# Performance work log

Hardware: AMD Instinct MI355X
Metric: run time of the kernel (lower is better)

The kernel has to match this reference:

```python
import jax, jax.numpy as jnp
import numpy as np

B, S, D, H = 32, 512, 512, 8
DH = D // H
EXP_FF, EXP_CONV, K = 4, 2, 31
EPS = 1e-5


def _layernorm(x, g, b):
    m = jnp.mean(x, axis=-1, keepdims=True)
    v = jnp.mean(jnp.square(x - m), axis=-1, keepdims=True)
    return (x - m) * jax.lax.rsqrt(v + EPS) * g + b


def _sinusoid_pe(s, d):
    pos = np.arange(s, dtype=np.float32)[:, None]
    i = np.arange(0, d, 2, dtype=np.float32)[None, :]
    ang = pos / np.power(10000.0, i / d)
    pe = np.zeros((s, d), dtype=np.float32)
    pe[:, 0::2] = np.sin(ang)
    pe[:, 1::2] = np.cos(ang)
    return jnp.asarray(pe)


def _rel_shift(ps):
    # Transformer-XL relative shift on [b,h,s,s]
    b, h, s1, s2 = ps.shape
    p = jnp.pad(ps, ((0, 0), (0, 0), (0, 0), (1, 0)))
    p = p.reshape(b, h, s2 + 1, s1)
    return p[:, :, 1:].reshape(b, h, s1, s2)


def setup_inputs() -> dict:
    key = jax.random.key(0)
    ks = iter(jax.random.split(key, 64))
    nrm = lambda shape, sc=0.02: jax.random.normal(next(ks), shape, jnp.float32) * sc
    ones = lambda n: jnp.ones((n,), jnp.float32)
    zeros = lambda n: jnp.zeros((n,), jnp.float32)
    return {
        'x': jax.random.normal(next(ks), (B, S, D), jnp.float32),
        'ff1_g': ones(D), 'ff1_b': zeros(D),
        'ff1_w1': nrm((D, EXP_FF * D)), 'ff1_b1': zeros(EXP_FF * D),
        'ff1_w2': nrm((EXP_FF * D, D)), 'ff1_b2': zeros(D),
        'attn_g': ones(D), 'attn_b': zeros(D),
        'wq': nrm((D, D)), 'bq': zeros(D),
        'wk': nrm((D, D)), 'bk': zeros(D),
        'wv': nrm((D, D)), 'bv': zeros(D),
        'wpos': nrm((D, D)),
        'u_bias': nrm((H, DH)), 'v_bias': nrm((H, DH)),
        'wo': nrm((D, D)), 'bo': zeros(D),
        'conv_g': ones(D), 'conv_b': zeros(D),
        'pw1_w': nrm((D, EXP_CONV * D)), 'pw1_b': zeros(EXP_CONV * D),
        'dw_w': nrm((D, 1, K)),
        'bn_g': ones(D), 'bn_b': zeros(D), 'bn_m': zeros(D), 'bn_v': ones(D),
        'pw2_w': nrm((D, D)), 'pw2_b': zeros(D),
        'ff2_g': ones(D), 'ff2_b': zeros(D),
        'ff2_w1': nrm((D, EXP_FF * D)), 'ff2_b1': zeros(EXP_FF * D),
        'ff2_w2': nrm((EXP_FF * D, D)), 'ff2_b2': zeros(D),
        'ln_g': ones(D), 'ln_b': zeros(D),
    }


def _ff(x, g, b, w1, b1, w2, b2):
    y = _layernorm(x, g, b)
    return jnp.dot(jax.nn.silu(jnp.dot(y, w1) + b1), w2) + b2


def reference(x, ff1_g, ff1_b, ff1_w1, ff1_b1, ff1_w2, ff1_b2,
              attn_g, attn_b, wq, bq, wk, bk, wv, bv, wpos, u_bias, v_bias, wo, bo,
              conv_g, conv_b, pw1_w, pw1_b, dw_w, bn_g, bn_b, bn_m, bn_v, pw2_w, pw2_b,
              ff2_g, ff2_b, ff2_w1, ff2_b1, ff2_w2, ff2_b2, ln_g, ln_b):
    b, s, d = x.shape
    # Macaron FF 1 (half-step residual)
    out = x + 0.5 * _ff(x, ff1_g, ff1_b, ff1_w1, ff1_b1, ff1_w2, ff1_b2)
    # Relative-position multi-head self-attention
    y = _layernorm(out, attn_g, attn_b)
    pe = _sinusoid_pe(s, d)
    q = (jnp.dot(y, wq) + bq).reshape(b, s, H, DH)
    k = (jnp.dot(y, wk) + bk).reshape(b, s, H, DH)
    v = (jnp.dot(y, wv) + bv).reshape(b, s, H, DH)
    p = jnp.dot(pe, wpos).reshape(s, H, DH)
    content = jnp.einsum('bqhd,bkhd->bhqk', q + u_bias, k)
    pos = _rel_shift(jnp.einsum('bqhd,khd->bhqk', q + v_bias, p))
    attn = jax.nn.softmax((content + pos) / np.sqrt(d).astype(np.float32), axis=-1)
    ctx = jnp.einsum('bhqk,bkhd->bqhd', attn, v).reshape(b, s, d)
    out = out + (jnp.dot(ctx, wo) + bo)
    y = _layernorm(out, conv_g, conv_b)
    y = jnp.dot(y, pw1_w) + pw1_b                     # [b,s,2d]
    a, gate = jnp.split(y, 2, axis=-1)
    y = (a * jax.nn.sigmoid(gate)).transpose(0, 2, 1)  # [b,d,s]
    pad = (K - 1) // 2
    y = jax.lax.conv_general_dilated(y, dw_w, (1,), [(pad, pad)],
                                     dimension_numbers=('NCH', 'OIH', 'NCH'),
                                     feature_group_count=d)
    y = (y - bn_m[None, :, None]) * jax.lax.rsqrt(bn_v + EPS)[None, :, None] \
        * bn_g[None, :, None] + bn_b[None, :, None]
    y = jax.nn.silu(y).transpose(0, 2, 1)             # [b,s,d]
    out = out + (jnp.dot(y, pw2_w) + pw2_b)
    # Macaron FF 2 + final LN
    out = out + 0.5 * _ff(out, ff2_g, ff2_b, ff2_w1, ff2_b1, ff2_w2, ff2_b2)
    out = _layernorm(out, ln_g, ln_b)
    return out, attn
```

## Files before the change

kernel.cpp:

```cpp
#include <hip/hip_runtime.h>
#include <cstddef>
#include <cstdint>

#define EPSF 1e-5f

constexpr int BB = 32, SS = 512, DD = 512, HH = 8, DH = 64;
constexpr int NTOK = BB * SS;
constexpr size_t ND = (size_t)NTOK * DD;

typedef __attribute__((ext_vector_type(8))) short bf16x8;
typedef __attribute__((ext_vector_type(4))) float f32x4;

__device__ __forceinline__ float sigmf(float v) { return 1.f / (1.f + __expf(-v)); }

__device__ __forceinline__ ushort f2bf(float f) {
  union { float f; uint32_t u; } x{f};
  uint32_t r = x.u + 0x7FFF + ((x.u >> 16) & 1);
  return (ushort)(r >> 16);
}
__device__ __forceinline__ float bf2f(ushort u) {
  union { uint32_t u; float f; } x{(uint32_t)u << 16};
  return x.f;
}

__device__ __forceinline__ void gload16(const ushort* g, ushort* ldsbase) {
  __builtin_amdgcn_global_load_lds((const __attribute__((address_space(1))) void*)g,
                                   (__attribute__((address_space(3))) void*)ldsbase, 16, 0, 0);
}

__device__ __forceinline__ void xcd_swz(int& bx, int& by) {
  const int gx = gridDim.x;
  const int nwg = gx * gridDim.y;
  const int cpx = nwg >> 3;
  int id = by * gx + bx;
  id = (id & 7) * cpx + (id >> 3);
  bx = id % gx;
  by = id / gx;
}

__device__ __forceinline__ int pswz(int idx) {
  return idx ^ (((idx >> 11) & 3) << 4);
}

__global__ __launch_bounds__(256) void ln_f32(const float* __restrict__ x,
                                              const float* __restrict__ g,
                                              const float* __restrict__ b,
                                              float* __restrict__ y) {
  const int lane = threadIdx.x & 63;
  const int row = blockIdx.x * 4 + (threadIdx.x >> 6);
  const float* xr = x + (size_t)row * 512;
  const float4 v0 = *(const float4*)&xr[lane << 2];
  const float4 v1 = *(const float4*)&xr[256 + (lane << 2)];
  float s = v0.x + v0.y + v0.z + v0.w + v1.x + v1.y + v1.z + v1.w;
#pragma unroll
  for (int o = 32; o > 0; o >>= 1) s += __shfl_xor(s, o);
  const float mean = s * (1.f / 512.f);
  float q = 0.f;
  q += (v0.x - mean) * (v0.x - mean); q += (v0.y - mean) * (v0.y - mean);
  q += (v0.z - mean) * (v0.z - mean); q += (v0.w - mean) * (v0.w - mean);
  q += (v1.x - mean) * (v1.x - mean); q += (v1.y - mean) * (v1.y - mean);
  q += (v1.z - mean) * (v1.z - mean); q += (v1.w - mean) * (v1.w - mean);
#pragma unroll
  for (int o = 32; o > 0; o >>= 1) q += __shfl_xor(q, o);
  const float rs = rsqrtf(q * (1.f / 512.f) + EPSF);
  const float4 g0 = *(const float4*)&g[lane << 2];
  const float4 g1 = *(const float4*)&g[256 + (lane << 2)];
  const float4 b0 = *(const float4*)&b[lane << 2];
  const float4 b1 = *(const float4*)&b[256 + (lane << 2)];
  float* yr = y + (size_t)row * 512;
  float4 o0, o1;
  o0.x = (v0.x - mean) * rs * g0.x + b0.x; o0.y = (v0.y - mean) * rs * g0.y + b0.y;
  o0.z = (v0.z - mean) * rs * g0.z + b0.z; o0.w = (v0.w - mean) * rs * g0.w + b0.w;
  o1.x = (v1.x - mean) * rs * g1.x + b1.x; o1.y = (v1.y - mean) * rs * g1.y + b1.y;
  o1.z = (v1.z - mean) * rs * g1.z + b1.z; o1.w = (v1.w - mean) * rs * g1.w + b1.w;
  *(float4*)&yr[lane << 2] = o0;
  *(float4*)&yr[256 + (lane << 2)] = o1;
}

__global__ __launch_bounds__(256) void ln_bf16(const float* __restrict__ x,
                                               const float* __restrict__ g,
                                               const float* __restrict__ b,
                                               ushort* __restrict__ y) {
  const int lane = threadIdx.x & 63;
  const int row = blockIdx.x * 4 + (threadIdx.x >> 6);
  const float* xr = x + (size_t)row * 512;
  const float4 v0 = *(const float4*)&xr[lane << 2];
  const float4 v1 = *(const float4*)&xr[256 + (lane << 2)];
  float s = v0.x + v0.y + v0.z + v0.w + v1.x + v1.y + v1.z + v1.w;
#pragma unroll
  for (int o = 32; o > 0; o >>= 1) s += __shfl_xor(s, o);
  const float mean = s * (1.f / 512.f);
  float q = 0.f;
  q += (v0.x - mean) * (v0.x - mean); q += (v0.y - mean) * (v0.y - mean);
  q += (v0.z - mean) * (v0.z - mean); q += (v0.w - mean) * (v0.w - mean);
  q += (v1.x - mean) * (v1.x - mean); q += (v1.y - mean) * (v1.y - mean);
  q += (v1.z - mean) * (v1.z - mean); q += (v1.w - mean) * (v1.w - mean);
#pragma unroll
  for (int o = 32; o > 0; o >>= 1) q += __shfl_xor(q, o);
  const float rs = rsqrtf(q * (1.f / 512.f) + EPSF);
  const float4 g0 = *(const float4*)&g[lane << 2];
  const float4 g1 = *(const float4*)&g[256 + (lane << 2)];
  const float4 b0 = *(const float4*)&b[lane << 2];
  const float4 b1 = *(const float4*)&b[256 + (lane << 2)];
  ushort* yr = y + (size_t)row * 512;
  ushort4 o0, o1;
  o0.x = f2bf((v0.x - mean) * rs * g0.x + b0.x); o0.y = f2bf((v0.y - mean) * rs * g0.y + b0.y);
  o0.z = f2bf((v0.z - mean) * rs * g0.z + b0.z); o0.w = f2bf((v0.w - mean) * rs * g0.w + b0.w);
  o1.x = f2bf((v1.x - mean) * rs * g1.x + b1.x); o1.y = f2bf((v1.y - mean) * rs * g1.y + b1.y);
  o1.z = f2bf((v1.z - mean) * rs * g1.z + b1.z); o1.w = f2bf((v1.w - mean) * rs * g1.w + b1.w);
  *(ushort4*)&yr[lane << 2] = o0;
  *(ushort4*)&yr[256 + (lane << 2)] = o1;
}

struct TpArgs {
  const float* src[11];
  ushort* dst[11];
  int K[11];
  int N[11];
  int base[12];
};

__global__ __launch_bounds__(256) void transpose_all(TpArgs a) {
  __shared__ float tile[32][33];
  int s = 0;
  const int bid = blockIdx.x;
  while (s < 10 && bid >= a.base[s + 1]) ++s;
  const int r = bid - a.base[s];
  const int K = a.K[s], N = a.N[s];
  const int ntx = N >> 5;
  const int n0 = (r % ntx) << 5;
  const int k0 = (r / ntx) << 5;
  const float* in = a.src[s];
  ushort* out = a.dst[s];
  const int tx = threadIdx.x & 31, ty = threadIdx.x >> 5;
#pragma unroll
  for (int i = 0; i < 32; i += 8)
    tile[ty + i][tx] = in[(size_t)(k0 + ty + i) * N + n0 + tx];
  __syncthreads();
#pragma unroll
  for (int i = 0; i < 32; i += 8)
    out[(size_t)(n0 + ty + i) * K + k0 + tx] = f2bf(tile[tx][ty + i]);
}

template <int ACT, int RES, int HB, int OBF>
__global__ __launch_bounds__(256) void gemm_bf16(const ushort* __restrict__ A,
                                                 const ushort* __restrict__ Wt,
                                                 const float* __restrict__ bias,
                                                 const float* __restrict__ res,
                                                 void* __restrict__ Cv,
                                                 int M, int K, int N) {
  __shared__ ushort Al[2][8192];
  __shared__ ushort Bl[2][8192];
  const int t = threadIdx.x;
  const int lane = t & 63;
  const int w = t >> 6;
  const int wr = (w >> 1) << 6, wc = (w & 1) << 6;
  int bx = blockIdx.x, by = blockIdx.y;
  xcd_swz(bx, by);
  const int m0 = by << 7, n0 = bx << 7;
  const int lm = lane & 15;
  const int grow = lane >> 3;
  const int gcol = (lane & 7) << 3;

  f32x4 acc[4][4];
#pragma unroll
  for (int i = 0; i < 4; ++i)
#pragma unroll
    for (int j = 0; j < 4; ++j) acc[i][j] = (f32x4)(0.f);

  const int NT = K >> 6;
#pragma unroll
  for (int i = 0; i < 4; ++i) {
    const int s = (w << 2) + i;
    gload16(A + (size_t)(m0 + (s << 3) + grow) * K + gcol, &Al[0][s << 9]);
    gload16(Wt + (size_t)(n0 + (s << 3) + grow) * K + gcol, &Bl[0][s << 9]);
  }
  __syncthreads();
  int cur = 0;
  for (int tt = 0; tt < NT; ++tt) {
    if (tt + 1 < NT) {
      const int k0 = (tt + 1) << 6;
#pragma unroll
      for (int i = 0; i < 4; ++i) {
        const int s = (w << 2) + i;
        gload16(A + (size_t)(m0 + (s << 3) + grow) * K + k0 + gcol, &Al[cur ^ 1][s << 9]);
        gload16(Wt + (size_t)(n0 + (s << 3) + grow) * K + k0 + gcol, &Bl[cur ^ 1][s << 9]);
      }
    }
#pragma unroll
    for (int ks = 0; ks < 2; ++ks) {
      const int kof = (ks << 5) + ((lane >> 4) << 3);
      bf16x8 af[4], bfr[4];
#pragma unroll
      for (int i = 0; i < 4; ++i) af[i] = *(const bf16x8*)&Al[cur][(wr + (i << 4) + lm) * 64 + kof];
#pragma unroll
      for (int j = 0; j < 4; ++j) bfr[j] = *(const bf16x8*)&Bl[cur][(wc + (j << 4) + lm) * 64 + kof];
#pragma unroll
      for (int i = 0; i < 4; ++i)
#pragma unroll
        for (int j = 0; j < 4; ++j)
          acc[i][j] = __builtin_amdgcn_mfma_f32_16x16x32_bf16(af[i], bfr[j], acc[i][j], 0, 0, 0);
    }
    __syncthreads();
    cur ^= 1;
  }

  float bb[4] = {0.f, 0.f, 0.f, 0.f};
  if (HB) {
#pragma unroll
    for (int j = 0; j < 4; ++j) bb[j] = bias[n0 + wc + j * 16 + lm];
  }
  const int rbase = m0 + wr + ((lane >> 4) << 2);
#pragma unroll
  for (int i = 0; i < 4; ++i) {
#pragma unroll
    for (int r = 0; r < 4; ++r) {
      const size_t row = (size_t)(rbase + i * 16 + r);
#pragma unroll
      for (int j = 0; j < 4; ++j) {
        const int col = n0 + wc + j * 16 + lm;
        float v = acc[i][j][r] + bb[j];
        if (ACT == 1) v = v * sigmf(v);
        if (RES == 1) v += res[row * N + col];
        else if (RES == 2) v = res[row * N + col] + 0.5f * v;
        if (OBF) ((ushort*)Cv)[row * N + col] = f2bf(v);
        else ((float*)Cv)[row * N + col] = v;
      }
    }
  }
}

__global__ __launch_bounds__(256) void gemm_qkv(const ushort* __restrict__ A,
                                                const ushort* __restrict__ Wt,
                                                const float* __restrict__ bq,
                                                const float* __restrict__ bk,
                                                const float* __restrict__ bv,
                                                const float* __restrict__ ub,
                                                const float* __restrict__ vb,
                                                ushort* __restrict__ qu,
                                                ushort* __restrict__ qv,
                                                ushort* __restrict__ kbb,
                                                ushort* __restrict__ vT,
                                                int M, int K) {
  __shared__ ushort Al[2][8192];
  __shared__ ushort Bl[2][8192];
  const int t = threadIdx.x;
  const int lane = t & 63;
  const int w = t >> 6;
  const int wr = (w >> 1) << 6, wc = (w & 1) << 6;
  int bx = blockIdx.x, by = blockIdx.y;
  xcd_swz(bx, by);
  const int m0 = by << 7, n0 = bx << 7;
  const int lm = lane & 15;
  const int grow = lane >> 3;
  const int gcol = (lane & 7) << 3;
  f32x4 acc[4][4];
#pragma unroll
  for (int i = 0; i < 4; ++i)
#pragma unroll
    for (int j = 0; j < 4; ++j) acc[i][j] = (f32x4)(0.f);
  const int NT = K >> 6;
#pragma unroll
  for (int i = 0; i < 4; ++i) {
    const int s = (w << 2) + i;
    gload16(A + (size_t)(m0 + (s << 3) + grow) * K + gcol, &Al[0][s << 9]);
    gload16(Wt + (size_t)(n0 + (s << 3) + grow) * K + gcol, &Bl[0][s << 9]);
  }
  __syncthreads();
  int cur = 0;
  for (int tt = 0; tt < NT; ++tt) {
    if (tt + 1 < NT) {
      const int k0 = (tt + 1) << 6;
#pragma unroll
      for (int i = 0; i < 4; ++i) {
        const int s = (w << 2) + i;
        gload16(A + (size_t)(m0 + (s << 3) + grow) * K + k0 + gcol, &Al[cur ^ 1][s << 9]);
        gload16(Wt + (size_t)(n0 + (s << 3) + grow) * K + k0 + gcol, &Bl[cur ^ 1][s << 9]);
      }
    }
#pragma unroll
    for (int ks = 0; ks < 2; ++ks) {
      const int kof = (ks << 5) + ((lane >> 4) << 3);
      bf16x8 af[4], bfr[4];
#pragma unroll
      for (int i = 0; i < 4; ++i) af[i] = *(const bf16x8*)&Al[cur][(wr + (i << 4) + lm) * 64 + kof];
#pragma unroll
      for (int j = 0; j < 4; ++j) bfr[j] = *(const bf16x8*)&Bl[cur][(wc + (j << 4) + lm) * 64 + kof];
#pragma unroll
      for (int i = 0; i < 4; ++i)
#pragma unroll
        for (int j = 0; j < 4; ++j)
          acc[i][j] = __builtin_amdgcn_mfma_f32_16x16x32_bf16(af[i], bfr[j], acc[i][j], 0, 0, 0);
    }
    __syncthreads();
    cur ^= 1;
  }
  const int seg = n0 >> 9;
  const int nloc = n0 & 511;
  const float* bsel = (seg == 0) ? bq : (seg == 1 ? bk : bv);
  float bb[4], uu[4], vv[4];
#pragma unroll
  for (int j = 0; j < 4; ++j) {
    const int col = nloc + wc + j * 16 + lm;
    bb[j] = bsel[col];
    if (seg == 0) { uu[j] = ub[col]; vv[j] = vb[col]; }
  }
  const int rbase = m0 + wr + ((lane >> 4) << 2);
  if (seg == 2) {
    const int bloc = m0 >> 9;
    const int sbase = rbase - (bloc << 9);
#pragma unroll
    for (int i = 0; i < 4; ++i) {
#pragma unroll
      for (int j = 0; j < 4; ++j) {
        const int col = nloc + wc + j * 16 + lm;
        ushort4 o;
        o.x = f2bf(acc[i][j][0] + bb[j]);
        o.y = f2bf(acc[i][j][1] + bb[j]);
        o.z = f2bf(acc[i][j][2] + bb[j]);
        o.w = f2bf(acc[i][j][3] + bb[j]);
        *(ushort4*)&vT[((size_t)((bloc << 9) + col)) * 512 + sbase + i * 16] = o;
      }
    }
    return;
  }
#pragma unroll
  for (int i = 0; i < 4; ++i) {
#pragma unroll
    for (int r = 0; r < 4; ++r) {
      const size_t row = (size_t)(rbase + i * 16 + r);
#pragma unroll
      for (int j = 0; j < 4; ++j) {
        const int col = nloc + wc + j * 16 + lm;
        const float v = acc[i][j][r] + bb[j];
        if (seg == 0) {
          qu[row * 512 + col] = f2bf(v + uu[j]);
          qv[row * 512 + col] = f2bf(v + vv[j]);
        } else {
          kbb[row * 512 + col] = f2bf(v);
        }
      }
    }
  }
}

__global__ __launch_bounds__(256) void gemm_glu(const ushort* __restrict__ A,
                                                const ushort* __restrict__ Wt,
                                                const float* __restrict__ bias,
                                                ushort* __restrict__ Cout,
                                                int M, int K) {
  __shared__ ushort Al[8192];
  __shared__ ushort Ba[8192];
  __shared__ ushort Bg[8192];
  const int t = threadIdx.x;
  const int lane = t & 63;
  const int w = t >> 6;
  const int wr = (w >> 1) << 6, wc = (w & 1) << 6;
  int bx = blockIdx.x, by = blockIdx.y;
  xcd_swz(bx, by);
  const int m0 = by << 7, n0 = bx << 7;
  const int lm = lane & 15;
  const int grow = lane >> 3;
  const int gcol = (lane & 7) << 3;
  const ushort* WtA = Wt;
  const ushort* WtG = Wt + (size_t)512 * 512;
  f32x4 acca[4][4], accg[4][4];
#pragma unroll
  for (int i = 0; i < 4; ++i)
#pragma unroll
    for (int j = 0; j < 4; ++j) { acca[i][j] = (f32x4)(0.f); accg[i][j] = (f32x4)(0.f); }
  const int NT = K >> 6;
  for (int tt = 0; tt < NT; ++tt) {
    const int k0 = tt << 6;
    if (tt) __syncthreads();
#pragma unroll
    for (int i = 0; i < 4; ++i) {
      const int s = (w << 2) + i;
      gload16(A + (size_t)(m0 + (s << 3) + grow) * K + k0 + gcol, &Al[s << 9]);
      gload16(WtA + (size_t)(n0 + (s << 3) + grow) * K + k0 + gcol, &Ba[s << 9]);
      gload16(WtG + (size_t)(n0 + (s << 3) + grow) * K + k0 + gcol, &Bg[s << 9]);
    }
    __syncthreads();
#pragma unroll
    for (int ks = 0; ks < 2; ++ks) {
      const int kof = (ks << 5) + ((lane >> 4) << 3);
      bf16x8 af[4], ba4[4], bg4[4];
#pragma unroll
      for (int i = 0; i < 4; ++i) af[i] = *(const bf16x8*)&Al[(wr + (i << 4) + lm) * 64 + kof];
#pragma unroll
      for (int j = 0; j < 4; ++j) {
        ba4[j] = *(const bf16x8*)&Ba[(wc + (j << 4) + lm) * 64 + kof];
        bg4[j] = *(const bf16x8*)&Bg[(wc + (j << 4) + lm) * 64 + kof];
      }
#pragma unroll
      for (int i = 0; i < 4; ++i)
#pragma unroll
        for (int j = 0; j < 4; ++j) {
          acca[i][j] = __builtin_amdgcn_mfma_f32_16x16x32_bf16(af[i], ba4[j], acca[i][j], 0, 0, 0);
          accg[i][j] = __builtin_amdgcn_mfma_f32_16x16x32_bf16(af[i], bg4[j], accg[i][j], 0, 0, 0);
        }
    }
  }
  float bba[4], bbg[4];
#pragma unroll
  for (int j = 0; j < 4; ++j) {
    const int col = n0 + wc + j * 16 + lm;
    bba[j] = bias[col];
    bbg[j] = bias[512 + col];
  }
  const int rbase = m0 + wr + ((lane >> 4) << 2);
#pragma unroll
  for (int i = 0; i < 4; ++i) {
#pragma unroll
    for (int r = 0; r < 4; ++r) {
      const size_t row = (size_t)(rbase + i * 16 + r);
#pragma unroll
      for (int j = 0; j < 4; ++j) {
        const int col = n0 + wc + j * 16 + lm;
        const float va = acca[i][j][r] + bba[j];
        const float vg = accg[i][j][r] + bbg[j];
        Cout[row * 512 + col] = f2bf(va * sigmf(vg));
      }
    }
  }
}

__global__ void pe_kernel_bf16(ushort* __restrict__ pe) {
  const int pos = blockIdx.x, ii = threadIdx.x;
  const float ang = (float)pos * powf(10000.f, -(float)(2 * ii) / 512.f);
  pe[((size_t)pos << 9) + 2 * ii] = f2bf(sinf(ang));
  pe[((size_t)pos << 9) + 2 * ii + 1] = f2bf(cosf(ang));
}

__global__ __launch_bounds__(256, 3) void attn_fused8(const ushort* __restrict__ qu,
                                                      const ushort* __restrict__ qv,
                                                      const ushort* __restrict__ kbb,
                                                      const ushort* __restrict__ ppb,
                                                      const ushort* __restrict__ vT,
                                                      float* __restrict__ attn,
                                                      ushort* __restrict__ ctx) {
  __shared__ ushort psl[17024];
  __shared__ union StU {
    struct { ushort p[2][32][72]; ushort k[2][32][72]; } pk;
    ushort v2[2][64][40];
    float scr[4][32];
    float scrC[2][64][17];
  } su;
  const int t = threadIdx.x, lane = t & 63, w = t >> 6;
  int bx = blockIdx.x, by = blockIdx.y;
  xcd_swz(bx, by);
  const int z = by, b = z >> 3, hh = z & 7;
  const int q0 = bx << 5;
  const int band = w >> 1, half = w & 1;
  const int lm = lane & 15, g = lane >> 4;
  const int lk = g << 3, fr4 = g << 2;
  const int C0 = half << 8;

  if (t < 33) {
    const int zi = t * 513 + 512;
    psl[pswz(zi)] = 0;
  }

  const size_t qoff = ((size_t)((b << 9) + q0 + (band << 4) + lm)) * 512 + (hh << 6);
  const bf16x8 av0 = *(const bf16x8*)&qv[qoff + lk];
  const bf16x8 av1 = *(const bf16x8*)&qv[qoff + lk + 32];
  const bf16x8 au0 = *(const bf16x8*)&qu[qoff + lk];
  const bf16x8 au1 = *(const bf16x8*)&qu[qoff + lk + 32];
  int er = q0 + 32 + lm;
  if (er > 511) er = 511;
  const size_t eoff = ((size_t)((b << 9) + er)) * 512 + (hh << 6);
  const bf16x8 e0 = *(const bf16x8*)&qv[eoff + lk];
  const bf16x8 e1 = *(const bf16x8*)&qv[eoff + lk + 32];

  const int srow = t >> 2, scg = (t & 3) << 4;
  const int sh = srow >> 5, sr = srow & 31;

  f32x4 acc[16];
#pragma unroll
  for (int i = 0; i < 16; ++i) acc[i] = (f32x4)(0.f);
  {
    const ushort* pb_ = ppb + (hh << 6);
    const ushort* kb_ = kbb + ((size_t)(b << 9)) * 512 + (hh << 6);
    const size_t off0 = (size_t)((sh << 8) + sr) * 512 + scg;
    bf16x8 rp0 = *(const bf16x8*)&pb_[off0];
    bf16x8 rp1 = *(const bf16x8*)&pb_[off0 + 8];
    bf16x8 rk0 = *(const bf16x8*)&kb_[off0];
    bf16x8 rk1 = *(const bf16x8*)&kb_[off0 + 8];
#pragma unroll
    for (int it = 0; it < 8; ++it) {
      __syncthreads();
      *(bf16x8*)&su.pk.p[sh][sr][scg] = rp0;
      *(bf16x8*)&su.pk.p[sh][sr][scg + 8] = rp1;
      *(bf16x8*)&su.pk.k[sh][sr][scg] = rk0;
      *(bf16x8*)&su.pk.k[sh][sr][scg + 8] = rk1;
      if (it < 7) {
        const size_t off = (size_t)((sh << 8) + ((it + 1) << 5) + sr) * 512 + scg;
        rp0 = *(const bf16x8*)&pb_[off];
        rp1 = *(const bf16x8*)&pb_[off + 8];
        rk0 = *(const bf16x8*)&kb_[off];
        rk1 = *(const bf16x8*)&kb_[off + 8];
      }
      __syncthreads();
      __builtin_amdgcn_s_setprio(1);
#pragma unroll
      for (int ctl = 0; ctl < 2; ++ctl) {
        {
          const bf16x8 b0 = *(const bf16x8*)&su.pk.p[half][(ctl << 4) + lm][lk];
          const bf16x8 b1 = *(const bf16x8*)&su.pk.p[half][(ctl << 4) + lm][32 + lk];
          f32x4 a = (f32x4)(0.f);
          a = __builtin_amdgcn_mfma_f32_16x16x32_bf16(av0, b0, a, 0, 0, 0);
          a = __builtin_amdgcn_mfma_f32_16x16x32_bf16(av1, b1, a, 0, 0, 0);
          const int col = C0 + (it << 5) + (ctl << 4) + lm;
#pragma unroll
          for (int r = 0; r < 4; ++r) {
            const int idx = ((band << 4) + fr4 + r) * 513 + col;
            psl[pswz(idx)] = f2bf(a[r]);
          }
          if (ctl == band) {
            f32x4 e = (f32x4)(0.f);
            e = __builtin_amdgcn_mfma_f32_16x16x32_bf16(e0, b0, e, 0, 0, 0);
            e = __builtin_amdgcn_mfma_f32_16x16x32_bf16(e1, b1, e, 0, 0, 0);
            if (g == 0) {
              const int idx = 32 * 513 + col;
              psl[pswz(idx)] = f2bf(e[0]);
            }
          }
        }
        {
          const int lct = (it << 1) + ctl;
          const bf16x8 b0 = *(const bf16x8*)&su.pk.k[half][(ctl << 4) + lm][lk];
          const bf16x8 b1 = *(const bf16x8*)&su.pk.k[half][(ctl << 4) + lm][32 + lk];
          acc[lct] = __builtin_amdgcn_mfma_f32_16x16x32_bf16(au0, b0, acc[lct], 0, 0, 0);
          acc[lct] = __builtin_amdgcn_mfma_f32_16x16x32_bf16(au1, b1, acc[lct], 0, 0, 0);
        }
      }
      __builtin_amdgcn_s_setprio(0);
    }
  }
  __syncthreads();

  const float scale = 0.044194173824159216f;
  const int qq0 = (band << 4) + fr4;
#pragma unroll
  for (int r = 0; r < 4; ++r) {
    const int qq = qq0 + r;
    const int pbase = qq * 512 + 511 - q0 + C0 + lm;
#pragma unroll
    for (int lct = 0; lct < 16; ++lct) {
      const float f = bf2f(psl[pswz(pbase + (lct << 4))]);
      acc[lct][r] = (acc[lct][r] + f) * scale;
    }
  }

  float mx[4] = {-3.0e38f, -3.0e38f, -3.0e38f, -3.0e38f};
#pragma unroll
  for (int lct = 0; lct < 16; ++lct)
#pragma unroll
    for (int r = 0; r < 4; ++r) mx[r] = fmaxf(mx[r], acc[lct][r]);
#pragma unroll
  for (int o = 1; o < 16; o <<= 1)
#pragma unroll
    for (int r = 0; r < 4; ++r) mx[r] = fmaxf(mx[r], __shfl_xor(mx[r], o));
  if (lm == 0) {
#pragma unroll
    for (int r = 0; r < 4; ++r) su.scr[half][qq0 + r] = mx[r];
  }
  __syncthreads();
#pragma unroll
  for (int r = 0; r < 4; ++r) mx[r] = fmaxf(mx[r], su.scr[half ^ 1][qq0 + r]);
  float sme[4] = {0.f, 0.f, 0.f, 0.f};
#pragma unroll
  for (int lct = 0; lct < 16; ++lct)
#pragma unroll
    for (int r = 0; r < 4; ++r) {
      acc[lct][r] = __expf(acc[lct][r] - mx[r]);
      sme[r] += acc[lct][r];
    }
#pragma unroll
  for (int o = 1; o < 16; o <<= 1)
#pragma unroll
    for (int r = 0; r < 4; ++r) sme[r] += __shfl_xor(sme[r], o);
  if (lm == 0) {
#pragma unroll
    for (int r = 0; r < 4; ++r) su.scr[2 + half][qq0 + r] = sme[r];
  }
  __syncthreads();
#pragma unroll
  for (int r = 0; r < 4; ++r) {
    const float inv = 1.f / (sme[r] + su.scr[2 + (half ^ 1)][qq0 + r]);
#pragma unroll
    for (int lct = 0; lct < 16; ++lct) acc[lct][r] *= inv;
  }
  __syncthreads();

  ushort* Pl = psl + ((band << 1) | half) * 736;
  const ushort* vtb = vT + ((size_t)((b << 9) + (hh << 6))) * 512;
  const int vrow = t >> 1, vc = (t & 1) << 4;
  const int vh = vrow >> 6, vd = vrow & 63;
  float* abase = attn + ((size_t)z << 18);
  f32x4 acc2[4];
#pragma unroll
  for (int i = 0; i < 4; ++i) acc2[i] = (f32x4)(0.f);
  bf16x8 p0 = *(const bf16x8*)&vtb[(size_t)vd * 512 + (vh << 8) + vc];
  bf16x8 p1 = *(const bf16x8*)&vtb[(size_t)vd * 512 + (vh << 8) + vc + 8];
#pragma unroll
  for (int ch = 0; ch < 8; ++ch) {
#pragma unroll
    for (int ctl = 0; ctl < 2; ++ctl) {
      const int lct = (ch << 1) + ctl;
#pragma unroll
      for (int r = 0; r < 4; ++r)
        Pl[(fr4 + r) * 46 + (ctl << 4) + lm] = f2bf(acc[lct][r]);
    }
    __syncthreads();
    *(bf16x8*)&su.v2[vh][vd][vc] = p0;
    *(bf16x8*)&su.v2[vh][vd][vc + 8] = p1;
    if (ch < 7) {
      const size_t off = (size_t)vd * 512 + (vh << 8) + ((ch + 1) << 5) + vc;
      p0 = *(const bf16x8*)&vtb[off];
      p1 = *(const bf16x8*)&vtb[off + 8];
    }
    {
      const int row = lane >> 2, colg = (lane & 3) << 3;
      const ushort* ps = Pl + row * 46 + colg;
      float* ar = abase + (size_t)(q0 + (band << 4) + row) * 512 + C0 + (ch << 5) + colg;
      float4 o0, o1;
      o0.x = bf2f(ps[0]); o0.y = bf2f(ps[1]); o0.z = bf2f(ps[2]); o0.w = bf2f(ps[3]);
      o1.x = bf2f(ps[4]); o1.y = bf2f(ps[5]); o1.z = bf2f(ps[6]); o1.w = bf2f(ps[7]);
      *(float4*)&ar[0] = o0;
      *(float4*)&ar[4] = o1;
    }
    __syncthreads();
    __builtin_amdgcn_s_setprio(1);
#pragma unroll
    for (int dt = 0; dt < 4; ++dt) {
      const bf16x8 va = *(const bf16x8*)&su.v2[half][(dt << 4) + lm][lk];
      const bf16x8 pbf = *(const bf16x8*)&Pl[lm * 46 + lk];
      acc2[dt] = __builtin_amdgcn_mfma_f32_16x16x32_bf16(va, pbf, acc2[dt], 0, 0, 0);
    }
    __builtin_amdgcn_s_setprio(0);
  }
  __syncthreads();
  if (half == 1) {
#pragma unroll
    for (int dt = 0; dt < 4; ++dt)
#pragma unroll
      for (int r = 0; r < 4; ++r)
        su.scrC[band][(dt << 4) + fr4 + r][lm] = acc2[dt][r];
  }
  __syncthreads();
  if (half == 0) {
    const int qq2 = q0 + (band << 4) + lm;
#pragma unroll
    for (int dt = 0; dt < 4; ++dt) {
      ushort4 o;
      o.x = f2bf(acc2[dt][0] + su.scrC[band][(dt << 4) + fr4 + 0][lm]);
      o.y = f2bf(acc2[dt][1] + su.scrC[band][(dt << 4) + fr4 + 1][lm]);
      o.z = f2bf(acc2[dt][2] + su.scrC[band][(dt << 4) + fr4 + 2][lm]);
      o.w = f2bf(acc2[dt][3] + su.scrC[band][(dt << 4) + fr4 + 3][lm]);
      *(ushort4*)&ctx[((size_t)((b << 9) + qq2)) * 512 + (hh << 6) + (dt << 4) + fr4] = o;
    }
  }
}

__global__ __launch_bounds__(256) void dwconv2(const ushort* __restrict__ in,
                                               const float* __restrict__ w,
                                               const float* __restrict__ bng,
                                               const float* __restrict__ bnb,
                                               const float* __restrict__ bnm,
                                               const float* __restrict__ bnv,
                                               ushort* __restrict__ out) {
  __shared__ float wl[31][128];
  const int t = threadIdx.x;
  const int dbase = blockIdx.x << 7;
  const int b = blockIdx.z;
  const int sb = (blockIdx.y << 6) + ((t >> 6) << 4);
  if (t < 128) {
    const float* ws = &w[(dbase + t) * 31];
#pragma unroll
    for (int k = 0; k < 31; ++k) wl[k][t] = ws[k];
  }
  __syncthreads();
  const int dl = (t & 63) << 1;
  const int d = dbase + dl;
  const size_t base = (((size_t)b) << 18) + d;
  float2 win[46];
#pragma unroll
  for (int i = 0; i < 46; ++i) {
    const int s = sb - 15 + i;
    if (s >= 0 && s < 512) {
      const ushort2 u = *(const ushort2*)&in[base + ((size_t)s << 9)];
      win[i].x = bf2f(u.x); win[i].y = bf2f(u.y);
    } else {
      win[i].x = 0.f; win[i].y = 0.f;
    }
  }
  float2 acc[16];
#pragma unroll
  for (int p = 0; p < 16; ++p) { acc[p].x = 0.f; acc[p].y = 0.f; }
#pragma unroll
  for (int k = 0; k < 31; ++k) {
    const float2 w2 = *(const float2*)&wl[k][dl];
#pragma unroll
    for (int p = 0; p < 16; ++p) {
      acc[p].x = fmaf(win[p + k].x, w2.x, acc[p].x);
      acc[p].y = fmaf(win[p + k].y, w2.y, acc[p].y);
    }
  }
  const float g0 = bng[d] * rsqrtf(bnv[d] + EPSF);
  const float g1 = bng[d + 1] * rsqrtf(bnv[d + 1] + EPSF);
  const float m0 = bnm[d], m1 = bnm[d + 1];
  const float bb0 = bnb[d], bb1 = bnb[d + 1];
#pragma unroll
  for (int p = 0; p < 16; ++p) {
    float v0 = (acc[p].x - m0) * g0 + bb0;
    float v1 = (acc[p].y - m1) * g1 + bb1;
    v0 = v0 * sigmf(v0);
    v1 = v1 * sigmf(v1);
    ushort2 o;
    o.x = f2bf(v0); o.y = f2bf(v1);
    *(ushort2*)&out[base + ((size_t)(sb + p) << 9)] = o;
  }
}

extern "C" void kernel_launch(void* const* d_in, const int* in_sizes, int n_in,
                              void* d_out, int out_size, void* d_ws, size_t ws_size,
                              hipStream_t stream) {
  const float* x      = (const float*)d_in[0];
  const float* ff1_g  = (const float*)d_in[1];
  const float* ff1_b  = (const float*)d_in[2];
  const float* ff1_w1 = (const float*)d_in[3];
  const float* ff1_b1 = (const float*)d_in[4];
  const float* ff1_w2 = (const float*)d_in[5];
  const float* ff1_b2 = (const float*)d_in[6];
  const float* attn_g = (const float*)d_in[7];
  const float* attn_b = (const float*)d_in[8];
  const float* wq     = (const float*)d_in[9];
  const float* bq     = (const float*)d_in[10];
  const float* wk     = (const float*)d_in[11];
  const float* bk     = (const float*)d_in[12];
  const float* wv     = (const float*)d_in[13];
  const float* bv     = (const float*)d_in[14];
  const float* wpos   = (const float*)d_in[15];
  const float* u_bias = (const float*)d_in[16];
  const float* v_bias = (const float*)d_in[17];
  const float* wo     = (const float*)d_in[18];
  const float* bo     = (const float*)d_in[19];
  const float* conv_g = (const float*)d_in[20];
  const float* conv_b = (const float*)d_in[21];
  const float* pw1_w  = (const float*)d_in[22];
  const float* pw1_b  = (const float*)d_in[23];
  const float* dw_w   = (const float*)d_in[24];
  const float* bn_g   = (const float*)d_in[25];
  const float* bn_b   = (const float*)d_in[26];
  const float* bn_m   = (const float*)d_in[27];
  const float* bn_v   = (const float*)d_in[28];
  const float* pw2_w  = (const float*)d_in[29];
  const float* pw2_b  = (const float*)d_in[30];
  const float* ff2_g  = (const float*)d_in[31];
  const float* ff2_b  = (const float*)d_in[32];
  const float* ff2_w1 = (const float*)d_in[33];
  const float* ff2_b1 = (const float*)d_in[34];
  const float* ff2_w2 = (const float*)d_in[35];
  const float* ff2_b2 = (const float*)d_in[36];
  const float* ln_g   = (const float*)d_in[37];
  const float* ln_b   = (const float*)d_in[38];

  float* out  = (float*)d_out;
  float* attn = out + ND;

  float*  res  = (float*)d_ws;
  ushort* ybf  = (ushort*)(res + ND);
  float*  big  = (float*)(ybf + ND);
  ushort* vT   = (ushort*)(big + 2 * ND);
  ushort* dwbf = vT + ND;
  ushort* wts  = dwbf + ND;
  ushort* pebf = wts + 6291456;
  ushort* ppbf = pebf + 262144;

  ushort* ffmid = (ushort*)big;
  ushort* qu    = (ushort*)big;
  ushort* qv    = qu + ND;
  ushort* kbb   = qv + ND;
  ushort* ctxbf = ybf;
  ushort* glubf = (ushort*)big;

  ushort* ff1w1t = wts;
  ushort* ff1w2t = wts + 1048576;
  ushort* wqt    = wts + 2097152;
  ushort* wkt    = wts + 2359296;
  ushort* wvt    = wts + 2621440;
  ushort* wot    = wts + 2883584;
  ushort* pw1t   = wts + 3145728;
  ushort* pw2t   = wts + 3670016;
  ushort* ff2w1t = wts + 3932160;
  ushort* ff2w2t = wts + 4980736;
  ushort* wpost  = wts + 6029312;

  const dim3 blk(256);

  TpArgs ta;
  auto set = [&](int i, const float* s, ushort* d, int K, int N) {
    ta.src[i] = s; ta.dst[i] = d; ta.K[i] = K; ta.N[i] = N;
  };
  set(0, ff1_w1, ff1w1t, 512, 2048);
  set(1, ff1_w2, ff1w2t, 2048, 512);
  set(2, wq, wqt, 512, 512);
  set(3, wk, wkt, 512, 512);
  set(4, wv, wvt, 512, 512);
  set(5, wo, wot, 512, 512);
  set(6, wpos, wpost, 512, 512);
  set(7, pw1_w, pw1t, 512, 1024);
  set(8, pw2_w, pw2t, 512, 512);
  set(9, ff2_w1, ff2w1t, 512, 2048);
  set(10, ff2_w2, ff2w2t, 2048, 512);
  int tacc = 0;
  for (int i = 0; i < 11; ++i) { ta.base[i] = tacc; tacc += (ta.N[i] >> 5) * (ta.K[i] >> 5); }
  ta.base[11] = tacc;
  transpose_all<<<tacc, blk, 0, stream>>>(ta);
  pe_kernel_bf16<<<512, blk, 0, stream>>>(pebf);
  gemm_bf16<0, 0, 0, 1><<<dim3(4, 4), blk, 0, stream>>>(pebf, wpost, nullptr, nullptr, ppbf,
                                                        512, 512, 512);

  ln_bf16<<<NTOK / 4, blk, 0, stream>>>(x, ff1_g, ff1_b, ybf);
  gemm_bf16<1, 0, 1, 1><<<dim3(16, 128), blk, 0, stream>>>(ybf, ff1w1t, ff1_b1, nullptr, ffmid,
                                                           NTOK, 512, 2048);
  gemm_bf16<0, 2, 1, 0><<<dim3(4, 128), blk, 0, stream>>>(ffmid, ff1w2t, ff1_b2, x, res,
                                                          NTOK, 2048, 512);

  ln_bf16<<<NTOK / 4, blk, 0, stream>>>(res, attn_g, attn_b, ybf);
  gemm_qkv<<<dim3(12, 128), blk, 0, stream>>>(ybf, wqt, bq, bk, bv, u_bias, v_bias,
                                              qu, qv, kbb, vT, NTOK, 512);
  attn_fused8<<<dim3(16, 256), blk, 0, stream>>>(qu, qv, kbb, ppbf, vT, attn, ctxbf);
  gemm_bf16<0, 1, 1, 0><<<dim3(4, 128), blk, 0, stream>>>(ctxbf, wot, bo, res, res,
                                                          NTOK, 512, 512);

  ln_bf16<<<NTOK / 4, blk, 0, stream>>>(res, conv_g, conv_b, ybf);
  gemm_glu<<<dim3(4, 128), blk, 0, stream>>>(ybf, pw1t, pw1_b, glubf, NTOK, 512);
  dwconv2<<<dim3(4, 8, 32), blk, 0, stream>>>(glubf, dw_w, bn_g, bn_b, bn_m, bn_v, dwbf);
  gemm_bf16<0, 1, 1, 0><<<dim3(4, 128), blk, 0, stream>>>(dwbf, pw2t, pw2_b, res, res,
                                                          NTOK, 512, 512);

  ln_bf16<<<NTOK / 4, blk, 0, stream>>>(res, ff2_g, ff2_b, ybf);
  gemm_bf16<1, 0, 1, 1><<<dim3(16, 128), blk, 0, stream>>>(ybf, ff2w1t, ff2_b1, nullptr, ffmid,
                                                           NTOK, 512, 2048);
  gemm_bf16<0, 2, 1, 0><<<dim3(4, 128), blk, 0, stream>>>(ffmid, ff2w2t, ff2_b2, res, res,
                                                          NTOK, 2048, 512);
  ln_f32<<<NTOK / 4, blk, 0, stream>>>(res, ln_g, ln_b, out);
}
```

Measured before the change: 718.6 us.

## Store residual stream in bf16 and widen attention P staging stride

The residual stream between sublayers is now kept as bf16 instead of fp32. GEMM epilogues read and write bf16 residuals, and new LayerNorm variants read bf16 input with 8-wide vector loads. This halves residual read/write traffic across the five residual GEMMs and four LayerNorms, at the cost of accumulating rounding error in the residual path. Separately, the attention kernel's LDS probability staging stride goes from 46 to 72 elements, so the attention-probability write-out can use a single 16-byte vector LDS read per lane.

```diff
diff --git a/kernel.cpp b/kernel.cpp
--- a/kernel.cpp
+++ b/kernel.cpp
@@ -42,41 +42,6 @@
   return idx ^ (((idx >> 11) & 3) << 4);
 }
 
-__global__ __launch_bounds__(256) void ln_f32(const float* __restrict__ x,
-                                              const float* __restrict__ g,
-                                              const float* __restrict__ b,
-                                              float* __restrict__ y) {
-  const int lane = threadIdx.x & 63;
-  const int row = blockIdx.x * 4 + (threadIdx.x >> 6);
-  const float* xr = x + (size_t)row * 512;
-  const float4 v0 = *(const float4*)&xr[lane << 2];
-  const float4 v1 = *(const float4*)&xr[256 + (lane << 2)];
-  float s = v0.x + v0.y + v0.z + v0.w + v1.x + v1.y + v1.z + v1.w;
-#pragma unroll
-  for (int o = 32; o > 0; o >>= 1) s += __shfl_xor(s, o);
-  const float mean = s * (1.f / 512.f);
-  float q = 0.f;
-  q += (v0.x - mean) * (v0.x - mean); q += (v0.y - mean) * (v0.y - mean);
-  q += (v0.z - mean) * (v0.z - mean); q += (v0.w - mean) * (v0.w - mean);
-  q += (v1.x - mean) * (v1.x - mean); q += (v1.y - mean) * (v1.y - mean);
-  q += (v1.z - mean) * (v1.z - mean); q += (v1.w - mean) * (v1.w - mean);
-#pragma unroll
-  for (int o = 32; o > 0; o >>= 1) q += __shfl_xor(q, o);
-  const float rs = rsqrtf(q * (1.f / 512.f) + EPSF);
-  const float4 g0 = *(const float4*)&g[lane << 2];
-  const float4 g1 = *(const float4*)&g[256 + (lane << 2)];
-  const float4 b0 = *(const float4*)&b[lane << 2];
-  const float4 b1 = *(const float4*)&b[256 + (lane << 2)];
-  float* yr = y + (size_t)row * 512;
-  float4 o0, o1;
-  o0.x = (v0.x - mean) * rs * g0.x + b0.x; o0.y = (v0.y - mean) * rs * g0.y + b0.y;
-  o0.z = (v0.z - mean) * rs * g0.z + b0.z; o0.w = (v0.w - mean) * rs * g0.w + b0.w;
-  o1.x = (v1.x - mean) * rs * g1.x + b1.x; o1.y = (v1.y - mean) * rs * g1.y + b1.y;
-  o1.z = (v1.z - mean) * rs * g1.z + b1.z; o1.w = (v1.w - mean) * rs * g1.w + b1.w;
-  *(float4*)&yr[lane << 2] = o0;
-  *(float4*)&yr[256 + (lane << 2)] = o1;
-}
-
 __global__ __launch_bounds__(256) void ln_bf16(const float* __restrict__ x,
                                                const float* __restrict__ g,
                                                const float* __restrict__ b,
@@ -84,32 +49,103 @@
   const int lane = threadIdx.x & 63;
   const int row = blockIdx.x * 4 + (threadIdx.x >> 6);
   const float* xr = x + (size_t)row * 512;
-  const float4 v0 = *(const float4*)&xr[lane << 2];
-  const float4 v1 = *(const float4*)&xr[256 + (lane << 2)];
-  float s = v0.x + v0.y + v0.z + v0.w + v1.x + v1.y + v1.z + v1.w;
+  const float4 v0 = *(const float4*)&xr[lane << 3];
+  const float4 v1 = *(const float4*)&xr[(lane << 3) + 4];
+  float f[8] = {v0.x, v0.y, v0.z, v0.w, v1.x, v1.y, v1.z, v1.w};
+  float s = 0.f;
+#pragma unroll
+  for (int k = 0; k < 8; ++k) s += f[k];
 #pragma unroll
   for (int o = 32; o > 0; o >>= 1) s += __shfl_xor(s, o);
   const float mean = s * (1.f / 512.f);
   float q = 0.f;
-  q += (v0.x - mean) * (v0.x - mean); q += (v0.y - mean) * (v0.y - mean);
-  q += (v0.z - mean) * (v0.z - mean); q += (v0.w - mean) * (v0.w - mean);
-  q += (v1.x - mean) * (v1.x - mean); q += (v1.y - mean) * (v1.y - mean);
-  q += (v1.z - mean) * (v1.z - mean); q += (v1.w - mean) * (v1.w - mean);
+#pragma unroll
+  for (int k = 0; k < 8; ++k) q += (f[k] - mean) * (f[k] - mean);
 #pragma unroll
   for (int o = 32; o > 0; o >>= 1) q += __shfl_xor(q, o);
   const float rs = rsqrtf(q * (1.f / 512.f) + EPSF);
-  const float4 g0 = *(const float4*)&g[lane << 2];
-  const float4 g1 = *(const float4*)&g[256 + (lane << 2)];
-  const float4 b0 = *(const float4*)&b[lane << 2];
-  const float4 b1 = *(const float4*)&b[256 + (lane << 2)];
-  ushort* yr = y + (size_t)row * 512;
-  ushort4 o0, o1;
-  o0.x = f2bf((v0.x - mean) * rs * g0.x + b0.x); o0.y = f2bf((v0.y - mean) * rs * g0.y + b0.y);
-  o0.z = f2bf((v0.z - mean) * rs * g0.z + b0.z); o0.w = f2bf((v0.w - mean) * rs * g0.w + b0.w);
-  o1.x = f2bf((v1.x - mean) * rs * g1.x + b1.x); o1.y = f2bf((v1.y - mean) * rs * g1.y + b1.y);
-  o1.z = f2bf((v1.z - mean) * rs * g1.z + b1.z); o1.w = f2bf((v1.w - mean) * rs * g1.w + b1.w);
-  *(ushort4*)&yr[lane << 2] = o0;
-  *(ushort4*)&yr[256 + (lane << 2)] = o1;
+  const float4 g0 = *(const float4*)&g[lane << 3];
+  const float4 g1 = *(const float4*)&g[(lane << 3) + 4];
+  const float4 b0 = *(const float4*)&b[lane << 3];
+  const float4 b1 = *(const float4*)&b[(lane << 3) + 4];
+  const float gg[8] = {g0.x, g0.y, g0.z, g0.w, g1.x, g1.y, g1.z, g1.w};
+  const float bb[8] = {b0.x, b0.y, b0.z, b0.w, b1.x, b1.y, b1.z, b1.w};
+  ushort tmp[8];
+#pragma unroll
+  for (int k = 0; k < 8; ++k) tmp[k] = f2bf((f[k] - mean) * rs * gg[k] + bb[k]);
+  *(bf16x8*)&y[(size_t)row * 512 + (lane << 3)] = *(bf16x8*)tmp;
+}
+
+__global__ __launch_bounds__(256) void lnb_bf16(const ushort* __restrict__ x,
+                                                const float* __restrict__ g,
+                                                const float* __restrict__ b,
+                                                ushort* __restrict__ y) {
+  const int lane = threadIdx.x & 63;
+  const int row = blockIdx.x * 4 + (threadIdx.x >> 6);
+  const bf16x8 v = *(const bf16x8*)&x[(size_t)row * 512 + (lane << 3)];
+  float f[8];
+#pragma unroll
+  for (int k = 0; k < 8; ++k) f[k] = bf2f((ushort)v[k]);
+  float s = 0.f;
+#pragma unroll
+  for (int k = 0; k < 8; ++k) s += f[k];
+#pragma unroll
+  for (int o = 32; o > 0; o >>= 1) s += __shfl_xor(s, o);
+  const float mean = s * (1.f / 512.f);
+  float q = 0.f;
+#pragma unroll
+  for (int k = 0; k < 8; ++k) q += (f[k] - mean) * (f[k] - mean);
+#pragma unroll
+  for (int o = 32; o > 0; o >>= 1) q += __shfl_xor(q, o);
+  const float rs = rsqrtf(q * (1.f / 512.f) + EPSF);
+  const float4 g0 = *(const float4*)&g[lane << 3];
+  const float4 g1 = *(const float4*)&g[(lane << 3) + 4];
+  const float4 b0 = *(const float4*)&b[lane << 3];
+  const float4 b1 = *(const float4*)&b[(lane << 3) + 4];
+  const float gg[8] = {g0.x, g0.y, g0.z, g0.w, g1.x, g1.y, g1.z, g1.w};
+  const float bb[8] = {b0.x, b0.y, b0.z, b0.w, b1.x, b1.y, b1.z, b1.w};
+  ushort tmp[8];
+#pragma unroll
+  for (int k = 0; k < 8; ++k) tmp[k] = f2bf((f[k] - mean) * rs * gg[k] + bb[k]);
+  *(bf16x8*)&y[(size_t)row * 512 + (lane << 3)] = *(bf16x8*)tmp;
+}
+
+__global__ __launch_bounds__(256) void lnb_f32(const ushort* __restrict__ x,
+                                               const float* __restrict__ g,
+                                               const float* __restrict__ b,
+                                               float* __restrict__ y) {
+  const int lane = threadIdx.x & 63;
+  const int row = blockIdx.x * 4 + (threadIdx.x >> 6);
+  const bf16x8 v = *(const bf16x8*)&x[(size_t)row * 512 + (lane << 3)];
+  float f[8];
+#pragma unroll
+  for (int k = 0; k < 8; ++k) f[k] = bf2f((ushort)v[k]);
+  float s = 0.f;
+#pragma unroll
+  for (int k = 0; k < 8; ++k) s += f[k];
+#pragma unroll
+  for (int o = 32; o > 0; o >>= 1) s += __shfl_xor(s, o);
+  const float mean = s * (1.f / 512.f);
+  float q = 0.f;
+#pragma unroll
+  for (int k = 0; k < 8; ++k) q += (f[k] - mean) * (f[k] - mean);
+#pragma unroll
+  for (int o = 32; o > 0; o >>= 1) q += __shfl_xor(q, o);
+  const float rs = rsqrtf(q * (1.f / 512.f) + EPSF);
+  const float4 g0 = *(const float4*)&g[lane << 3];
+  const float4 g1 = *(const float4*)&g[(lane << 3) + 4];
+  const float4 b0 = *(const float4*)&b[lane << 3];
+  const float4 b1 = *(const float4*)&b[(lane << 3) + 4];
+  const float gg[8] = {g0.x, g0.y, g0.z, g0.w, g1.x, g1.y, g1.z, g1.w};
+  const float bb[8] = {b0.x, b0.y, b0.z, b0.w, b1.x, b1.y, b1.z, b1.w};
+  float* yr = y + (size_t)row * 512 + (lane << 3);
+  float4 o0, o1;
+  o0.x = (f[0] - mean) * rs * gg[0] + bb[0]; o0.y = (f[1] - mean) * rs * gg[1] + bb[1];
+  o0.z = (f[2] - mean) * rs * gg[2] + bb[2]; o0.w = (f[3] - mean) * rs * gg[3] + bb[3];
+  o1.x = (f[4] - mean) * rs * gg[4] + bb[4]; o1.y = (f[5] - mean) * rs * gg[5] + bb[5];
+  o1.z = (f[6] - mean) * rs * gg[6] + bb[6]; o1.w = (f[7] - mean) * rs * gg[7] + bb[7];
+  *(float4*)&yr[0] = o0;
+  *(float4*)&yr[4] = o1;
 }
 
 struct TpArgs {
@@ -142,11 +178,11 @@
     out[(size_t)(n0 + ty + i) * K + k0 + tx] = f2bf(tile[tx][ty + i]);
 }
 
-template <int ACT, int RES, int HB, int OBF>
+template <int ACT, int RES, int HB, int OBF, int RSRC>
 __global__ __launch_bounds__(256) void gemm_bf16(const ushort* __restrict__ A,
                                                  const ushort* __restrict__ Wt,
                                                  const float* __restrict__ bias,
-                                                 const float* __restrict__ res,
+                                                 const void* __restrict__ res,
                                                  void* __restrict__ Cv,
                                                  int M, int K, int N) {
   __shared__ ushort Al[2][8192];
@@ -221,8 +257,12 @@
         const int col = n0 + wc + j * 16 + lm;
         float v = acc[i][j][r] + bb[j];
         if (ACT == 1) v = v * sigmf(v);
-        if (RES == 1) v += res[row * N + col];
-        else if (RES == 2) v = res[row * N + col] + 0.5f * v;
+        if (RES == 1 || RES == 2) {
+          float rv;
+          if (RSRC) rv = bf2f(((const ushort*)res)[row * N + col]);
+          else rv = ((const float*)res)[row * N + col];
+          v = (RES == 1) ? (rv + v) : (rv + 0.5f * v);
+        }
         if (OBF) ((ushort*)Cv)[row * N + col] = f2bf(v);
         else ((float*)Cv)[row * N + col] = v;
       }
@@ -432,7 +472,7 @@
   pe[((size_t)pos << 9) + 2 * ii + 1] = f2bf(cosf(ang));
 }
 
-__global__ __launch_bounds__(256, 3) void attn_fused8(const ushort* __restrict__ qu,
+__global__ __launch_bounds__(256, 3) void attn_fused9(const ushort* __restrict__ qu,
                                                       const ushort* __restrict__ qv,
                                                       const ushort* __restrict__ kbb,
                                                       const ushort* __restrict__ ppb,
@@ -593,7 +633,7 @@
   }
   __syncthreads();
 
-  ushort* Pl = psl + ((band << 1) | half) * 736;
+  ushort* Pl = psl + ((band << 1) | half) * 1152;
   const ushort* vtb = vT + ((size_t)((b << 9) + (hh << 6))) * 512;
   const int vrow = t >> 1, vc = (t & 1) << 4;
   const int vh = vrow >> 6, vd = vrow & 63;
@@ -610,7 +650,7 @@
       const int lct = (ch << 1) + ctl;
 #pragma unroll
       for (int r = 0; r < 4; ++r)
-        Pl[(fr4 + r) * 46 + (ctl << 4) + lm] = f2bf(acc[lct][r]);
+        Pl[(fr4 + r) * 72 + (ctl << 4) + lm] = f2bf(acc[lct][r]);
     }
     __syncthreads();
     *(bf16x8*)&su.v2[vh][vd][vc] = p0;
@@ -622,11 +662,13 @@
     }
     {
       const int row = lane >> 2, colg = (lane & 3) << 3;
-      const ushort* ps = Pl + row * 46 + colg;
+      const bf16x8 pv8 = *(const bf16x8*)&Pl[row * 72 + colg];
       float* ar = abase + (size_t)(q0 + (band << 4) + row) * 512 + C0 + (ch << 5) + colg;
       float4 o0, o1;
-      o0.x = bf2f(ps[0]); o0.y = bf2f(ps[1]); o0.z = bf2f(ps[2]); o0.w = bf2f(ps[3]);
-      o1.x = bf2f(ps[4]); o1.y = bf2f(ps[5]); o1.z = bf2f(ps[6]); o1.w = bf2f(ps[7]);
+      o0.x = bf2f((ushort)pv8[0]); o0.y = bf2f((ushort)pv8[1]);
+      o0.z = bf2f((ushort)pv8[2]); o0.w = bf2f((ushort)pv8[3]);
+      o1.x = bf2f((ushort)pv8[4]); o1.y = bf2f((ushort)pv8[5]);
+      o1.z = bf2f((ushort)pv8[6]); o1.w = bf2f((ushort)pv8[7]);
       *(float4*)&ar[0] = o0;
       *(float4*)&ar[4] = o1;
     }
@@ -635,7 +677,7 @@
 #pragma unroll
     for (int dt = 0; dt < 4; ++dt) {
       const bf16x8 va = *(const bf16x8*)&su.v2[half][(dt << 4) + lm][lk];
-      const bf16x8 pbf = *(const bf16x8*)&Pl[lm * 46 + lk];
+      const bf16x8 pbf = *(const bf16x8*)&Pl[lm * 72 + lk];
       acc2[dt] = __builtin_amdgcn_mfma_f32_16x16x32_bf16(va, pbf, acc2[dt], 0, 0, 0);
     }
     __builtin_amdgcn_s_setprio(0);
@@ -769,8 +811,8 @@
   float* out  = (float*)d_out;
   float* attn = out + ND;
 
-  float*  res  = (float*)d_ws;
-  ushort* ybf  = (ushort*)(res + ND);
+  ushort* resb = (ushort*)d_ws;
+  ushort* ybf  = resb + ND;
   float*  big  = (float*)(ybf + ND);
   ushort* vT   = (ushort*)(big + 2 * ND);
   ushort* dwbf = vT + ND;
@@ -819,32 +861,32 @@
   ta.base[11] = tacc;
   transpose_all<<<tacc, blk, 0, stream>>>(ta);
   pe_kernel_bf16<<<512, blk, 0, stream>>>(pebf);
-  gemm_bf16<0, 0, 0, 1><<<dim3(4, 4), blk, 0, stream>>>(pebf, wpost, nullptr, nullptr, ppbf,
-                                                        512, 512, 512);
+  gemm_bf16<0, 0, 0, 1, 0><<<dim3(4, 4), blk, 0, stream>>>(pebf, wpost, nullptr, nullptr, ppbf,
+                                                           512, 512, 512);
 
   ln_bf16<<<NTOK / 4, blk, 0, stream>>>(x, ff1_g, ff1_b, ybf);
-  gemm_bf16<1, 0, 1, 1><<<dim3(16, 128), blk, 0, stream>>>(ybf, ff1w1t, ff1_b1, nullptr, ffmid,
-                                                           NTOK, 512, 2048);
-  gemm_bf16<0, 2, 1, 0><<<dim3(4, 128), blk, 0, stream>>>(ffmid, ff1w2t, ff1_b2, x, res,
-                                                          NTOK, 2048, 512);
-
-  ln_bf16<<<NTOK / 4, blk, 0, stream>>>(res, attn_g, attn_b, ybf);
+  gemm_bf16<1, 0, 1, 1, 0><<<dim3(16, 128), blk, 0, stream>>>(ybf, ff1w1t, ff1_b1, nullptr,
+                                                              ffmid, NTOK, 512, 2048);
+  gemm_bf16<0, 2, 1, 1, 0><<<dim3(4, 128), blk, 0, stream>>>(ffmid, ff1w2t, ff1_b2, x, resb,
+                                                             NTOK, 2048, 512);
+
+  lnb_bf16<<<NTOK / 4, blk, 0, stream>>>(resb, attn_g, attn_b, ybf);
   gemm_qkv<<<dim3(12, 128), blk, 0, stream>>>(ybf, wqt, bq, bk, bv, u_bias, v_bias,
                                               qu, qv, kbb, vT, NTOK, 512);
-  attn_fused8<<<dim3(16, 256), blk, 0, stream>>>(qu, qv, kbb, ppbf, vT, attn, ctxbf);
-  gemm_bf16<0, 1, 1, 0><<<dim3(4, 128), blk, 0, stream>>>(ctxbf, wot, bo, res, res,
-                                                          NTOK, 512, 512);
-
-  ln_bf16<<<NTOK / 4, blk, 0, stream>>>(res, conv_g, conv_b, ybf);
+  attn_fused9<<<dim3(16, 256), blk, 0, stream>>>(qu, qv, kbb, ppbf, vT, attn, ctxbf);
+  gemm_bf16<0, 1, 1, 1, 1><<<dim3(4, 128), blk, 0, stream>>>(ctxbf, wot, bo, resb, resb,
+                                                             NTOK, 512, 512);
+
+  lnb_bf16<<<NTOK / 4, blk, 0, stream>>>(resb, conv_g, conv_b, ybf);
   gemm_glu<<<dim3(4, 128), blk, 0, stream>>>(ybf, pw1t, pw1_b, glubf, NTOK, 512);
   dwconv2<<<dim3(4, 8, 32), blk, 0, stream>>>(glubf, dw_w, bn_g, bn_b, bn_m, bn_v, dwbf);
-  gemm_bf16<0, 1, 1, 0><<<dim3(4, 128), blk, 0, stream>>>(dwbf, pw2t, pw2_b, res, res,
-                                                          NTOK, 512, 512);
-
-  ln_bf16<<<NTOK / 4, blk, 0, stream>>>(res, ff2_g, ff2_b, ybf);
-  gemm_bf16<1, 0, 1, 1><<<dim3(16, 128), blk, 0, stream>>>(ybf, ff2w1t, ff2_b1, nullptr, ffmid,
-                                                           NTOK, 512, 2048);
-  gemm_bf16<0, 2, 1, 0><<<dim3(4, 128), blk, 0, stream>>>(ffmid, ff2w2t, ff2_b2, res, res,
-                                                          NTOK, 2048, 512);
-  ln_f32<<<NTOK / 4, blk, 0, stream>>>(res, ln_g, ln_b, out);
-}
+  gemm_bf16<0, 1, 1, 1, 1><<<dim3(4, 128), blk, 0, stream>>>(dwbf, pw2t, pw2_b, resb, resb,
+                                                             NTOK, 512, 512);
+
+  lnb_bf16<<<NTOK / 4, blk, 0, stream>>>(resb, ff2_g, ff2_b, ybf);
+  gemm_bf16<1, 0, 1, 1, 0><<<dim3(16, 128), blk, 0, stream>>>(ybf, ff2w1t, ff2_b1, nullptr,
+                                                              ffmid, NTOK, 512, 2048);
+  gemm_bf16<0, 2, 1, 1, 1><<<dim3(4, 128), blk, 0, stream>>>(ffmid, ff2w2t, ff2_b2, resb, resb,
+                                                             NTOK, 2048, 512);
+  lnb_f32<<<NTOK / 4, blk, 0, stream>>>(resb, ln_g, ln_b, out);
+}
```

Result: faster. 693.4 us (-3.5%).
